# Kernel tuning notes

Hardware: AMD Instinct MI355X
Metric: run time of the kernel (lower is better)

The kernel has to match this reference:

```python
import jax, jax.numpy as jnp
import numpy as np

NUM_HEADS = 16


def setup_inputs() -> dict:
    key = jax.random.key(0)
    ks = jax.random.split(key, 10)
    B, T, D = 2, 2048, 1024
    s = D ** -0.5  # keep activations O(1)
    return {
        "inputs": jax.random.normal(ks[0], (B, T, D), dtype=jnp.float32),
        "mask": jax.random.randint(ks[1], (B, T, T), 0, 2, dtype=jnp.int32),
        "Wq": jax.random.normal(ks[2], (D, D), dtype=jnp.float32) * s,
        "bq": jnp.zeros((D,), dtype=jnp.float32),
        "Wk": jax.random.normal(ks[3], (D, D), dtype=jnp.float32) * s,
        "bk": jnp.zeros((D,), dtype=jnp.float32),
        "Wv": jax.random.normal(ks[4], (D, D), dtype=jnp.float32) * s,
        "bv": jnp.zeros((D,), dtype=jnp.float32),
        "Wo": jax.random.normal(ks[5], (D, D), dtype=jnp.float32) * s,
        "bo": jnp.zeros((D,), dtype=jnp.float32),
    }


def _split_heads(x, h):
    # [B,T,D] -> [B,H,T,D/H]
    B, T, D = x.shape
    return x.reshape(B, T, h, D // h).transpose(0, 2, 1, 3)


def reference(inputs, mask, Wq, bq, Wk, bk, Wv, bv, Wo, bo):
    B, T, D = inputs.shape
    H = NUM_HEADS
    dh = D // H
    q = _split_heads(inputs @ Wq + bq, H) * (dh ** -0.5)  # [B,H,T,dh]
    k = _split_heads(inputs @ Wk + bk, H)
    v = _split_heads(inputs @ Wv + bv, H)
    dot = jnp.einsum("bhqd,bhkd->bhqk", q, k)  # [B,H,T,T]
    m = mask.astype(jnp.float32)[:, None]  # [B,1,T,T]
    dot = dot * m + (1.0 - m) * jnp.finfo(jnp.float32).min
    attn = jax.nn.softmax(dot, axis=-1)
    # dropout inactive at inference (training=False)
    heads = jnp.einsum("bhqk,bhkd->bhqd", attn, v)
    combined = heads.transpose(0, 2, 1, 3).reshape(B, T, D)
    return combined @ Wo + bo
```

## Files before the change

kernel.cpp:

```cpp
#include <hip/hip_runtime.h>
#include <hip/hip_bf16.h>
#include <stdint.h>

typedef _Float16 f16;
typedef __attribute__((ext_vector_type(8))) _Float16 f16x8;
typedef __attribute__((ext_vector_type(2))) __fp16 fp16x2;
typedef __attribute__((ext_vector_type(4))) float f32x4;
typedef __attribute__((ext_vector_type(16))) float f32x16;

#define B_  2
#define T_  2048
#define D_  1024
#define H_  16
#define DH_ 64
#define NSPLIT 2
#define KVSPAN (T_ / NSPLIT)

__device__ __forceinline__ f32x4 mfma16f(f16x8 a, f16x8 b, f32x4 c) {
    return __builtin_amdgcn_mfma_f32_16x16x32_f16(a, b, c, 0, 0, 0);
}
__device__ __forceinline__ f32x16 mfma32f(f16x8 a, f16x8 b, f32x16 c) {
    return __builtin_amdgcn_mfma_f32_32x32x16_f16(a, b, c, 0, 0, 0);
}
__device__ __forceinline__ void gload16(const void* g, void* l) {
    __builtin_amdgcn_global_load_lds(
        (const __attribute__((address_space(1))) uint32_t*)g,
        (__attribute__((address_space(3))) uint32_t*)l, 16, 0, 0);
}
__device__ __forceinline__ float xmax32(float x) {
    float a, b;
    asm("v_mov_b32 %0, %2\n\t"
        "v_mov_b32 %1, %2\n\t"
        "s_nop 1\n\t"
        "v_permlane32_swap_b32 %0, %1\n\t"
        "s_nop 1\n\t"
        "v_max_f32 %0, %0, %1"
        : "=&v"(a), "=&v"(b) : "v"(x));
    return a;
}
__device__ __forceinline__ float xsum32(float x) {
    float a, b;
    asm("v_mov_b32 %0, %2\n\t"
        "v_mov_b32 %1, %2\n\t"
        "s_nop 1\n\t"
        "v_permlane32_swap_b32 %0, %1\n\t"
        "s_nop 1\n\t"
        "v_add_f32 %0, %0, %1"
        : "=&v"(a), "=&v"(b) : "v"(x));
    return a;
}

__global__ __launch_bounds__(256) void maskpack_kernel(
    const int* __restrict__ mask, uint32_t* __restrict__ bitsT)
{
    size_t e = (size_t)blockIdx.x * 256 + threadIdx.x;
    unsigned long long bb = __ballot(mask[e] != 0);
    if ((threadIdx.x & 63) == 0) {
        size_t r = e >> 11;
        int b = (int)(r >> 11), q = (int)(r & (T_ - 1));
        int k = (int)(e & (T_ - 1));
        int w0 = k >> 5;
        size_t base = (size_t)b * (64 * T_) + q;
        bitsT[base + (size_t)w0 * T_]       = (uint32_t)bb;
        bitsT[base + (size_t)(w0 + 1) * T_] = (uint32_t)(bb >> 32);
    }
}

__global__ __launch_bounds__(256) void cvtx_kernel(
    const float* __restrict__ X, f16* __restrict__ Xh)
{
    size_t i0 = ((size_t)blockIdx.x * 256 + threadIdx.x) * 8;
    float4 a = *(const float4*)(X + i0);
    float4 b = *(const float4*)(X + i0 + 4);
    float v[8] = {a.x, a.y, a.z, a.w, b.x, b.y, b.z, b.w};
    f16x8 hh;
#pragma unroll
    for (int i = 0; i < 8; ++i) hh[i] = (f16)v[i];
    *(f16x8*)(Xh + i0) = hh;
}

__global__ __launch_bounds__(256) void wtr_kernel(
    const float* __restrict__ Wq, const float* __restrict__ Wk,
    const float* __restrict__ Wv, const float* __restrict__ Wo,
    f16* __restrict__ WqT, f16* __restrict__ WkT,
    f16* __restrict__ WvT, f16* __restrict__ WoT)
{
    __shared__ float s_t[64][65];
    const int zz = blockIdx.z;
    const float* __restrict__ W = (zz == 0) ? Wq : (zz == 1) ? Wk : (zz == 2) ? Wv : Wo;
    const int k0 = blockIdx.y * 64, n0 = blockIdx.x * 64;
    const int t = threadIdx.x;
    const int r = t >> 2, c0 = (t & 3) * 16;

#pragma unroll
    for (int j = 0; j < 4; ++j) {
        float4 v = *(const float4*)(W + (size_t)(k0 + r) * D_ + n0 + c0 + j * 4);
        s_t[r][c0 + j * 4 + 0] = v.x;
        s_t[r][c0 + j * 4 + 1] = v.y;
        s_t[r][c0 + j * 4 + 2] = v.z;
        s_t[r][c0 + j * 4 + 3] = v.w;
    }
    __syncthreads();

    const int n = t >> 2, kc = (t & 3) * 16;
    f16x8 h0, h1;
#pragma unroll
    for (int j = 0; j < 8; ++j) h0[j] = (f16)s_t[kc + j][n];
#pragma unroll
    for (int j = 0; j < 8; ++j) h1[j] = (f16)s_t[kc + 8 + j][n];
    f16* dh = (zz == 0) ? WqT : (zz == 1) ? WkT : (zz == 2) ? WvT : WoT;
    size_t o = (size_t)(n0 + n) * D_ + k0 + kc;
    *(f16x8*)(dh + o) = h0;
    *(f16x8*)(dh + o + 8) = h1;
}

__global__ __launch_bounds__(256) void gemm_kernel(
    const f16* __restrict__ A, int zbase,
    const f16* __restrict__ BqT, const f16* __restrict__ BkT,
    const f16* __restrict__ BvT, const f16* __restrict__ BoT,
    const float* __restrict__ bq, const float* __restrict__ bk,
    const float* __restrict__ bv, const float* __restrict__ bo,
    f16* __restrict__ Q, f16* __restrict__ K,
    f16* __restrict__ Vt, float* __restrict__ outF)
{
    __shared__ f16 sA[128 * 32];
    __shared__ f16 sB[128 * 32];

    const int z = blockIdx.z + zbase;
    const f16* __restrict__ Bm = (z == 0) ? BqT : (z == 1) ? BkT : (z == 2) ? BvT : BoT;
    const float* __restrict__ bias = (z == 0) ? bq : (z == 1) ? bk : (z == 2) ? bv : bo;

    const int m0 = blockIdx.y * 128;
    const int n0 = blockIdx.x * 128;
    const int tid = threadIdx.x;
    const int w = tid >> 6, l = tid & 63;
    const int g = l >> 4, lr = l & 15;
    const int wm = w >> 1, wn = w & 1;

    const int srow = w * 32 + (l >> 2);
    const int skb  = (l & 3) * 8;

    f32x4 acc[4][4] = {};

    for (int k0 = 0; k0 < D_; k0 += 32) {
        __syncthreads();
#pragma unroll
        for (int i = 0; i < 2; ++i) {
            gload16(A  + (size_t)(m0 + srow + i * 16) * D_ + k0 + skb,
                    &sA[w * 1024 + i * 512]);
            gload16(Bm + (size_t)(n0 + srow + i * 16) * D_ + k0 + skb,
                    &sB[w * 1024 + i * 512]);
        }
        __syncthreads();

        f16x8 ah[4], bh[4];
#pragma unroll
        for (int f = 0; f < 4; ++f) {
            ah[f] = *(const f16x8*)&sA[(wm * 64 + f * 16 + lr) * 32 + g * 8];
            bh[f] = *(const f16x8*)&sB[(wn * 64 + f * 16 + lr) * 32 + g * 8];
        }
#pragma unroll
        for (int fm = 0; fm < 4; ++fm)
#pragma unroll
            for (int fn = 0; fn < 4; ++fn)
                acc[fm][fn] = mfma16f(ah[fm], bh[fn], acc[fm][fn]);
    }

    const float scale = (z == 0) ? 0.125f : 1.0f;
    float biasv[4];
#pragma unroll
    for (int f = 0; f < 4; ++f) biasv[f] = bias[n0 + wn * 64 + f * 16 + lr];

    if (z <= 1) {
        f16* Oq = (z == 0) ? Q : K;
#pragma unroll
        for (int fm = 0; fm < 4; ++fm)
#pragma unroll
            for (int fn = 0; fn < 4; ++fn)
#pragma unroll
                for (int j = 0; j < 4; ++j) {
                    int r = m0 + wm * 64 + fm * 16 + g * 4 + j;
                    int c = n0 + wn * 64 + fn * 16 + lr;
                    float v = (acc[fm][fn][j] + biasv[fn]) * scale;
                    int b = r >> 11, t = r & (T_ - 1);
                    int h = (c >> 6) & 15, d = c & 63;
                    Oq[((size_t)(b * H_ + h) * T_ + t) * DH_ + d] = (f16)v;
                }
    } else if (z == 2) {
#pragma unroll
        for (int fm = 0; fm < 4; ++fm)
#pragma unroll
            for (int fn = 0; fn < 4; ++fn) {
                int r0 = m0 + wm * 64 + fm * 16 + g * 4;
                int c  = n0 + wn * 64 + fn * 16 + lr;
                int b = r0 >> 11, t0 = r0 & (T_ - 1);
                int h = (c >> 6) & 15, d = c & 63;
                union { f16 h4[4]; uint2 u; } pk;
#pragma unroll
                for (int j = 0; j < 4; ++j)
                    pk.h4[j] = (f16)(acc[fm][fn][j] + biasv[fn]);
                *(uint2*)&Vt[(size_t)(b * H_ + h) * (T_ * DH_) +
                             (size_t)(t0 >> 5) * (32 * DH_) + d * 32 + (t0 & 31)] = pk.u;
            }
    } else {
#pragma unroll
        for (int fm = 0; fm < 4; ++fm)
#pragma unroll
            for (int fn = 0; fn < 4; ++fn)
#pragma unroll
                for (int j = 0; j < 4; ++j) {
                    int r = m0 + wm * 64 + fm * 16 + g * 4 + j;
                    int c = n0 + wn * 64 + fn * 16 + lr;
                    outF[(size_t)r * D_ + c] = acc[fm][fn][j] + biasv[fn];
                }
    }
}

__device__ __forceinline__ void attn_tile(
    const f16x8* kh, const f16x8* vb, uint32_t mw, const f16x8* qf,
    f32x16& o0, f32x16& o1, float& m_run, float& l_run)
{
    const float L2E = 1.4426950408889634f;
    f32x16 s = {};
    __builtin_amdgcn_s_setprio(1);
    s = mfma32f(kh[0], qf[0], s);
    s = mfma32f(kh[1], qf[1], s);
    s = mfma32f(kh[2], qf[2], s);
    s = mfma32f(kh[3], qf[3], s);
    __builtin_amdgcn_s_setprio(0);

#pragma unroll
    for (int r = 0; r < 16; ++r) {
        const int bit = (r & 3) + 8 * (r >> 2);
        if (!((mw >> bit) & 1u)) s[r] = -1e30f;
    }

    float t8[8], t4[4];
#pragma unroll
    for (int i = 0; i < 8; ++i) t8[i] = fmaxf(s[i], s[i + 8]);
#pragma unroll
    for (int i = 0; i < 4; ++i) t4[i] = fmaxf(t8[i], t8[i + 4]);
    float pm = fmaxf(fmaxf(t4[0], t4[2]), fmaxf(t4[1], t4[3]));
    pm = xmax32(pm);

    if (__any(pm > m_run + 8.0f)) {
        float mn  = fmaxf(m_run, pm);
        float fac = exp2f((m_run - mn) * L2E);
        l_run *= fac;
#pragma unroll
        for (int r = 0; r < 16; ++r) { o0[r] *= fac; o1[r] *= fac; }
        m_run = mn;
    }

    float p[16];
#pragma unroll
    for (int r = 0; r < 16; ++r) p[r] = exp2f((s[r] - m_run) * L2E);
    float a8[8], a4[4];
#pragma unroll
    for (int i = 0; i < 8; ++i) a8[i] = p[i] + p[i + 8];
#pragma unroll
    for (int i = 0; i < 4; ++i) a4[i] = a8[i] + a8[i + 4];
    float sum = (a4[0] + a4[2]) + (a4[1] + a4[3]);
    sum = xsum32(sum);
    l_run += sum;

    uint32_t wv[8];
#pragma unroll
    for (int m2 = 0; m2 < 8; ++m2) {
        union { fp16x2 h; uint32_t u; } cv;
        cv.h = __builtin_amdgcn_cvt_pkrtz(p[2 * m2], p[2 * m2 + 1]);
        wv[m2] = cv.u;
    }
    asm("v_permlane32_swap_b32 %0, %1" : "+v"(wv[0]), "+v"(wv[2]));
    asm("v_permlane32_swap_b32 %0, %1" : "+v"(wv[1]), "+v"(wv[3]));
    asm("v_permlane32_swap_b32 %0, %1" : "+v"(wv[4]), "+v"(wv[6]));
    asm("v_permlane32_swap_b32 %0, %1" : "+v"(wv[5]), "+v"(wv[7]));
    union { uint32_t u[4]; f16x8 s8; } pa1, pa2;
    pa1.u[0] = wv[0]; pa1.u[1] = wv[1]; pa1.u[2] = wv[2]; pa1.u[3] = wv[3];
    pa2.u[0] = wv[4]; pa2.u[1] = wv[5]; pa2.u[2] = wv[6]; pa2.u[3] = wv[7];

    __builtin_amdgcn_s_setprio(1);
    o0 = mfma32f(vb[0], pa1.s8, o0);
    o0 = mfma32f(vb[1], pa2.s8, o0);
    o1 = mfma32f(vb[2], pa1.s8, o1);
    o1 = mfma32f(vb[3], pa2.s8, o1);
    __builtin_amdgcn_s_setprio(0);
}

__global__ __launch_bounds__(256, 3) void attn_split_kernel(
    const f16* __restrict__ Qg, const f16* __restrict__ Kg,
    const f16* __restrict__ Vt, const uint32_t* __restrict__ bits,
    f16* __restrict__ Op0, f16* __restrict__ Op1,
    float2* __restrict__ stats)
{
    __shared__ f16 sK[2][2048];
    __shared__ f16 sV[2][2048];

    const int bx  = blockIdx.x;
    const int bh  = (bx & 7) | ((bx >> 8) << 3);
    const int mid = (bx >> 3) & 31;
    const int qb  = mid >> 1;
    const int sp  = mid & 1;
    const int b   = bh >> 4, h = bh & 15;
    const int tid = threadIdx.x;
    const int w   = tid >> 6;
    const int l   = tid & 63;
    const int qi  = l & 31;
    const int hl  = l >> 5;
    const int q   = qb * 128 + w * 32 + qi;
    const int kvbase = sp * KVSPAN;

    const size_t hoff = (size_t)(b * H_ + h) * T_ * DH_;
    const f16* Qh = Qg + hoff;
    const f16* Kh = Kg + hoff;
    const f16* Vh = Vt + hoff;
    const uint32_t* mbase = bits + (size_t)b * (64 * T_) + q;

    const int krow = tid >> 3, kch = tid & 7;
    const size_t ksoff = (size_t)krow * DH_ + (size_t)((kch ^ (krow & 7)) * 8);
    const int vrow = tid >> 2, vch = tid & 3;
    const size_t vsoff = (size_t)vrow * 32 + (size_t)((vch ^ ((vrow >> 1) & 3)) * 8);

    f16x8 qf[4];
#pragma unroll
    for (int c = 0; c < 4; ++c)
        qf[c] = *(const f16x8*)&Qh[(size_t)q * DH_ + c * 16 + hl * 8];

    f32x16 o0 = {}; f32x16 o1 = {};
    float m_run = -1e30f, l_run = 0.0f;

#define STAGE(buf, kv)                                                        \
    do {                                                                      \
        gload16(Kh + (size_t)(kv) * DH_ + ksoff, &sK[buf][w * 512]);          \
        gload16(Vh + (size_t)((kv) >> 5) * 2048 + vsoff, &sV[buf][w * 512]);  \
    } while (0)

    STAGE(0, kvbase);
    __syncthreads();

    int cur = 0;
    for (int kv0 = kvbase; kv0 < kvbase + KVSPAN; kv0 += 32) {
        int nxt = kv0 + 32;
        if (nxt == kvbase + KVSPAN) nxt = kvbase;
        STAGE(cur ^ 1, nxt);

        uint32_t mw = mbase[(size_t)(kv0 >> 5) * T_] >> (hl * 4);

        f16x8 kh[4], vb[4];
#pragma unroll
        for (int c = 0; c < 4; ++c)
            kh[c] = *(const f16x8*)&sK[cur][qi * DH_ + (((2 * c + hl) ^ (qi & 7)) << 3)];
#pragma unroll
        for (int j = 0; j < 4; ++j) {
            int row = (j >> 1) * 32 + qi;
            int ch  = ((j & 1) * 2 + hl) ^ ((qi >> 1) & 3);
            vb[j] = *(const f16x8*)&sV[cur][row * 32 + (ch << 3)];
        }

        attn_tile(kh, vb, mw, qf, o0, o1, m_run, l_run);
        __syncthreads();
        cur ^= 1;
    }
#undef STAGE

    float inv = 1.0f / l_run;
    float ov[32];
#pragma unroll
    for (int r = 0; r < 16; ++r) { ov[r] = o0[r]; ov[16 + r] = o1[r]; }
    f16* Op = (sp == 0) ? Op0 : Op1;
    f16* prow = Op + ((size_t)bh * T_ + q) * DH_;
#pragma unroll
    for (int dt = 0; dt < 2; ++dt)
#pragma unroll
        for (int g2 = 0; g2 < 4; ++g2) {
            union { f16 h4[4]; uint2 u; } pk;
#pragma unroll
            for (int j = 0; j < 4; ++j)
                pk.h4[j] = (f16)(ov[dt * 16 + 4 * g2 + j] * inv);
            *(uint2*)(prow + dt * 32 + 8 * g2 + 4 * hl) = pk.u;
        }
    if (hl == 0)
        stats[(size_t)sp * (32 * T_) + (size_t)bh * T_ + q] =
            make_float2(m_run, l_run);
}

__global__ __launch_bounds__(256) void combine_kernel(
    const f16* __restrict__ Op0, const f16* __restrict__ Op1,
    const float2* __restrict__ stats, f16* __restrict__ comb)
{
    const float L2E = 1.4426950408889634f;
    const int row = blockIdx.x * 32 + (threadIdx.x >> 3);
    const int dh0 = (threadIdx.x & 7) * 8;
    const int bh = row >> 11, q = row & (T_ - 1);
    const int b = bh >> 4, h = bh & 15;

    float2 s0 = stats[row];
    float2 s1 = stats[32 * T_ + row];
    float m = fmaxf(s0.x, s1.x);
    float w0 = s0.y * exp2f((s0.x - m) * L2E);
    float w1 = s1.y * exp2f((s1.x - m) * L2E);
    float rs = 1.0f / (w0 + w1);
    float a0 = w0 * rs, a1 = w1 * rs;

    f16x8 v0 = *(const f16x8*)(Op0 + (size_t)row * DH_ + dh0);
    f16x8 v1 = *(const f16x8*)(Op1 + (size_t)row * DH_ + dh0);
    f16x8 ou;
#pragma unroll
    for (int i = 0; i < 8; ++i)
        ou[i] = (f16)(a0 * (float)v0[i] + a1 * (float)v1[i]);
    *(f16x8*)(comb + ((size_t)(b * T_ + q)) * D_ + h * DH_ + dh0) = ou;
}

extern "C" void kernel_launch(void* const* d_in, const int* in_sizes, int n_in,
                              void* d_out, int out_size, void* d_ws, size_t ws_size,
                              hipStream_t stream)
{
    const float* X    = (const float*)d_in[0];
    const int*   mask = (const int*)d_in[1];
    const float* Wq   = (const float*)d_in[2];
    const float* bq   = (const float*)d_in[3];
    const float* Wk   = (const float*)d_in[4];
    const float* bk   = (const float*)d_in[5];
    const float* Wv   = (const float*)d_in[6];
    const float* bv   = (const float*)d_in[7];
    const float* Wo   = (const float*)d_in[8];
    const float* bo   = (const float*)d_in[9];
    float* out = (float*)d_out;

    const size_t SEG  = (size_t)B_ * T_ * D_;
    const size_t WSEG = (size_t)D_ * D_;
    f16* wsp = (f16*)d_ws;
    f16* Q    = wsp + 0 * SEG;
    f16* K    = wsp + 1 * SEG;
    f16* Xh   = wsp + 2 * SEG;
    f16* Op0  = wsp + 3 * SEG;
    f16* WqT  = wsp + 4 * SEG;
    f16* WkT  = WqT + 1 * WSEG;
    f16* WvT  = WqT + 2 * WSEG;
    f16* WoT  = WqT + 3 * WSEG;
    f16* Op1  = wsp + 5 * SEG;
    f16* comb = Xh;
    f16* Vt = (f16*)d_out;
    uint32_t* bits = (uint32_t*)((char*)d_out + (8u << 20));
    float2* stats  = (float2*)((char*)d_out + (9u << 20));

    dim3 blk(256);
    maskpack_kernel<<<dim3((B_ * T_ * T_) / 256), blk, 0, stream>>>(mask, bits);
    cvtx_kernel<<<dim3((B_ * T_ * D_) / 2048), blk, 0, stream>>>(X, Xh);
    wtr_kernel<<<dim3(16, 16, 4), blk, 0, stream>>>(
        Wq, Wk, Wv, Wo, WqT, WkT, WvT, WoT);
    gemm_kernel<<<dim3(D_ / 128, (B_ * T_) / 128, 3), blk, 0, stream>>>(
        Xh, 0, WqT, WkT, WvT, WoT,
        bq, bk, bv, bo, Q, K, Vt, out);
    attn_split_kernel<<<dim3(B_ * H_ * (T_ / 128) * NSPLIT), blk, 0, stream>>>(
        Q, K, Vt, bits, Op0, Op1, stats);
    combine_kernel<<<dim3((32 * T_) / 32), blk, 0, stream>>>(
        Op0, Op1, stats, comb);
    gemm_kernel<<<dim3(D_ / 128, (B_ * T_) / 128, 1), blk, 0, stream>>>(
        comb, 3, WqT, WkT, WvT, WoT,
        bq, bk, bv, bo, Q, K, Vt, out);
}
```

Baseline: 161.7 us.

## Double-buffer GEMM LDS staging and split output projection into smaller-tile kernel

Result: slower. 184.7 us (+14.2%).

```diff
diff --git a/kernel.cpp b/kernel.cpp
--- a/kernel.cpp
+++ b/kernel.cpp
@@ -115,20 +115,19 @@
 }
 
 __global__ __launch_bounds__(256) void gemm_kernel(
-    const f16* __restrict__ A, int zbase,
+    const f16* __restrict__ A,
     const f16* __restrict__ BqT, const f16* __restrict__ BkT,
-    const f16* __restrict__ BvT, const f16* __restrict__ BoT,
+    const f16* __restrict__ BvT,
     const float* __restrict__ bq, const float* __restrict__ bk,
-    const float* __restrict__ bv, const float* __restrict__ bo,
-    f16* __restrict__ Q, f16* __restrict__ K,
-    f16* __restrict__ Vt, float* __restrict__ outF)
-{
-    __shared__ f16 sA[128 * 32];
-    __shared__ f16 sB[128 * 32];
-
-    const int z = blockIdx.z + zbase;
-    const f16* __restrict__ Bm = (z == 0) ? BqT : (z == 1) ? BkT : (z == 2) ? BvT : BoT;
-    const float* __restrict__ bias = (z == 0) ? bq : (z == 1) ? bk : (z == 2) ? bv : bo;
+    const float* __restrict__ bv,
+    f16* __restrict__ Q, f16* __restrict__ K, f16* __restrict__ Vt)
+{
+    __shared__ f16 sA[2][128 * 32];
+    __shared__ f16 sB[2][128 * 32];
+
+    const int z = blockIdx.z;
+    const f16* __restrict__ Bm = (z == 0) ? BqT : (z == 1) ? BkT : BvT;
+    const float* __restrict__ bias = (z == 0) ? bq : (z == 1) ? bk : bv;
 
     const int m0 = blockIdx.y * 128;
     const int n0 = blockIdx.x * 128;
@@ -142,29 +141,39 @@
 
     f32x4 acc[4][4] = {};
 
+#define GSTAGE(buf, kk)                                                        \
+    do {                                                                       \
+        _Pragma("unroll")                                                      \
+        for (int i = 0; i < 2; ++i) {                                          \
+            gload16(A  + (size_t)(m0 + srow + i * 16) * D_ + (kk) + skb,       \
+                    &sA[buf][w * 1024 + i * 512]);                             \
+            gload16(Bm + (size_t)(n0 + srow + i * 16) * D_ + (kk) + skb,       \
+                    &sB[buf][w * 1024 + i * 512]);                             \
+        }                                                                      \
+    } while (0)
+
+    GSTAGE(0, 0);
+    __syncthreads();
+    int cur = 0;
     for (int k0 = 0; k0 < D_; k0 += 32) {
-        __syncthreads();
-#pragma unroll
-        for (int i = 0; i < 2; ++i) {
-            gload16(A  + (size_t)(m0 + srow + i * 16) * D_ + k0 + skb,
-                    &sA[w * 1024 + i * 512]);
-            gload16(Bm + (size_t)(n0 + srow + i * 16) * D_ + k0 + skb,
-                    &sB[w * 1024 + i * 512]);
-        }
-        __syncthreads();
+        if (k0 + 32 < D_) GSTAGE(cur ^ 1, k0 + 32);
 
         f16x8 ah[4], bh[4];
 #pragma unroll
         for (int f = 0; f < 4; ++f) {
-            ah[f] = *(const f16x8*)&sA[(wm * 64 + f * 16 + lr) * 32 + g * 8];
-            bh[f] = *(const f16x8*)&sB[(wn * 64 + f * 16 + lr) * 32 + g * 8];
+            ah[f] = *(const f16x8*)&sA[cur][(wm * 64 + f * 16 + lr) * 32 + g * 8];
+            bh[f] = *(const f16x8*)&sB[cur][(wn * 64 + f * 16 + lr) * 32 + g * 8];
         }
 #pragma unroll
         for (int fm = 0; fm < 4; ++fm)
 #pragma unroll
             for (int fn = 0; fn < 4; ++fn)
                 acc[fm][fn] = mfma16f(ah[fm], bh[fn], acc[fm][fn]);
-    }
+
+        __syncthreads();
+        cur ^= 1;
+    }
+#undef GSTAGE
 
     const float scale = (z == 0) ? 0.125f : 1.0f;
     float biasv[4];
@@ -186,7 +195,7 @@
                     int h = (c >> 6) & 15, d = c & 63;
                     Oq[((size_t)(b * H_ + h) * T_ + t) * DH_ + d] = (f16)v;
                 }
-    } else if (z == 2) {
+    } else {
 #pragma unroll
         for (int fm = 0; fm < 4; ++fm)
 #pragma unroll
@@ -202,18 +211,75 @@
                 *(uint2*)&Vt[(size_t)(b * H_ + h) * (T_ * DH_) +
                              (size_t)(t0 >> 5) * (32 * DH_) + d * 32 + (t0 & 31)] = pk.u;
             }
-    } else {
-#pragma unroll
-        for (int fm = 0; fm < 4; ++fm)
+    }
+}
+
+__global__ __launch_bounds__(256) void oproj_kernel(
+    const f16* __restrict__ A, const f16* __restrict__ BoT,
+    const float* __restrict__ bo, float* __restrict__ outF)
+{
+    __shared__ f16 sA[2][128 * 32];
+    __shared__ f16 sB[2][64 * 32];
+
+    const int m0 = blockIdx.y * 128;
+    const int n0 = blockIdx.x * 64;
+    const int tid = threadIdx.x;
+    const int w = tid >> 6, l = tid & 63;
+    const int g = l >> 4, lr = l & 15;
+
+    const int srowA = w * 32 + (l >> 2);
+    const int skbA  = (l & 3) * 8;
+    const int browB = w * 16 + (l >> 2);
+
+    f32x4 acc[2][4] = {};
+
+#define OSTAGE(buf, kk)                                                        \
+    do {                                                                       \
+        _Pragma("unroll")                                                      \
+        for (int i = 0; i < 2; ++i)                                            \
+            gload16(A + (size_t)(m0 + srowA + i * 16) * D_ + (kk) + skbA,      \
+                    &sA[buf][w * 1024 + i * 512]);                             \
+        gload16(BoT + (size_t)(n0 + browB) * D_ + (kk) + skbA,                 \
+                &sB[buf][w * 512]);                                            \
+    } while (0)
+
+    OSTAGE(0, 0);
+    __syncthreads();
+    int cur = 0;
+    for (int k0 = 0; k0 < D_; k0 += 32) {
+        if (k0 + 32 < D_) OSTAGE(cur ^ 1, k0 + 32);
+
+        f16x8 ah[2], bh[4];
+#pragma unroll
+        for (int f = 0; f < 2; ++f)
+            ah[f] = *(const f16x8*)&sA[cur][(w * 32 + f * 16 + lr) * 32 + g * 8];
+#pragma unroll
+        for (int f = 0; f < 4; ++f)
+            bh[f] = *(const f16x8*)&sB[cur][(f * 16 + lr) * 32 + g * 8];
+#pragma unroll
+        for (int fm = 0; fm < 2; ++fm)
 #pragma unroll
             for (int fn = 0; fn < 4; ++fn)
-#pragma unroll
-                for (int j = 0; j < 4; ++j) {
-                    int r = m0 + wm * 64 + fm * 16 + g * 4 + j;
-                    int c = n0 + wn * 64 + fn * 16 + lr;
-                    outF[(size_t)r * D_ + c] = acc[fm][fn][j] + biasv[fn];
-                }
-    }
+                acc[fm][fn] = mfma16f(ah[fm], bh[fn], acc[fm][fn]);
+
+        __syncthreads();
+        cur ^= 1;
+    }
+#undef OSTAGE
+
+    float biasv[4];
+#pragma unroll
+    for (int f = 0; f < 4; ++f) biasv[f] = bo[n0 + f * 16 + lr];
+#pragma unroll
+    for (int fm = 0; fm < 2; ++fm)
+#pragma unroll
+        for (int fn = 0; fn < 4; ++fn)
+#pragma unroll
+            for (int j = 0; j < 4; ++j) {
+                int r = m0 + w * 32 + fm * 16 + g * 4 + j;
+                int c = n0 + fn * 16 + lr;
+                outF[(size_t)r * D_ + c] = acc[fm][fn][j] + biasv[fn];
+            }
 }
 
 __device__ __forceinline__ void attn_tile(
@@ -450,13 +516,11 @@
     wtr_kernel<<<dim3(16, 16, 4), blk, 0, stream>>>(
         Wq, Wk, Wv, Wo, WqT, WkT, WvT, WoT);
     gemm_kernel<<<dim3(D_ / 128, (B_ * T_) / 128, 3), blk, 0, stream>>>(
-        Xh, 0, WqT, WkT, WvT, WoT,
-        bq, bk, bv, bo, Q, K, Vt, out);
+        Xh, WqT, WkT, WvT, bq, bk, bv, Q, K, Vt);
     attn_split_kernel<<<dim3(B_ * H_ * (T_ / 128) * NSPLIT), blk, 0, stream>>>(
         Q, K, Vt, bits, Op0, Op1, stats);
     combine_kernel<<<dim3((32 * T_) / 32), blk, 0, stream>>>(
         Op0, Op1, stats, comb);
-    gemm_kernel<<<dim3(D_ / 128, (B_ * T_) / 128, 1), blk, 0, stream>>>(
-        comb, 3, WqT, WkT, WvT, WoT,
-        bq, bk, bv, bo, Q, K, Vt, out);
-}
+    oproj_kernel<<<dim3(D_ / 64, (B_ * T_) / 128), blk, 0, stream>>>(
+        comb, WoT, bo, out);
+}
```
